# Kernel optimization log

Measured on AMD Instinct MI355X. Metric: run time of the kernel, lower is better.

## Reference

```python
import jax, jax.numpy as jnp
import numpy as np

D = 256      # d_model
H = 8        # num heads
HD = D // H  # head dim
DFF = 1024   # feedforward dim
S = 1024     # seq len
B = 8        # batch
EPS = 1e-5


def _layernorm(x, g, b):
    mu = jnp.mean(x, axis=-1, keepdims=True)
    var = jnp.mean((x - mu) ** 2, axis=-1, keepdims=True)
    return (x - mu) * jax.lax.rsqrt(var + EPS) * g + b


def setup_inputs() -> dict:
    key = jax.random.key(0)
    ks = jax.random.split(key, 12)
    xav = lambda k, shape: jax.random.uniform(
        k, shape, jnp.float32, -1.0, 1.0) * np.sqrt(6.0 / (shape[0] + shape[-1]))
    return {
        "src": jax.random.normal(ks[0], (S, B, D), jnp.float32),
        "bias": jax.random.normal(ks[1], (B, H, S, S), jnp.float32),
        "in_proj_w": xav(ks[2], (3 * D, D)),
        "in_proj_b": jnp.zeros((3 * D,), jnp.float32),
        "out_w": xav(ks[3], (D, D)),
        "out_b": jnp.zeros((D,), jnp.float32),
        "w1": xav(ks[4], (DFF, D)),
        "b1": jnp.zeros((DFF,), jnp.float32),
        "w2": xav(ks[5], (D, DFF)),
        "b2": jnp.zeros((D,), jnp.float32),
        "g1": jnp.ones((D,), jnp.float32),
        "be1": jnp.zeros((D,), jnp.float32),
        "g2": jnp.ones((D,), jnp.float32),
        "be2": jnp.zeros((D,), jnp.float32),
    }


def reference(src, bias, in_proj_w, in_proj_b, out_w, out_b,
              w1, b1, w2, b2, g1, be1, g2, be2):
    # Pre-norm (note: residual uses the NORMED src, matching the torch code)
    x = _layernorm(src, g1, be1)                       # [S,B,D]
    qkv = x @ in_proj_w.T + in_proj_b                  # [S,B,3D]
    q, k, v = jnp.split(qkv, 3, axis=-1)
    q = q * (HD ** -0.5)
    # [S,B,D] -> [B,H,S,HD]
    to_heads = lambda t: t.reshape(S, B, H, HD).transpose(1, 2, 0, 3)
    qh, kh, vh = to_heads(q), to_heads(k), to_heads(v)
    scores = jnp.einsum('bhsd,bhtd->bhst', qh, kh) + bias
    attn = jax.nn.softmax(scores, axis=-1)             # [B,H,S,S]
    ctx = jnp.einsum('bhst,bhtd->bhsd', attn, vh)      # [B,H,S,HD]
    ctx = ctx.transpose(2, 0, 1, 3).reshape(S, B, D)
    attn_out = ctx @ out_w.T + out_b
    x = x + attn_out                                   # residual (eval: no dropout)
    y = _layernorm(x, g2, be2)
    ff = jax.nn.relu(y @ w1.T + b1) @ w2.T + b2
    return y + ff
```

## Files before the change

### kernel.cpp

```cpp
#include <hip/hip_runtime.h>
#include <hip/hip_bf16.h>
#include <cstdint>

typedef unsigned short u16;
typedef __attribute__((ext_vector_type(8))) short bf16x8;
typedef __attribute__((ext_vector_type(4))) float f32x4;

#define S_LEN 1024
#define BATCH 8
#define DMODEL 256
#define NHEAD 8
#define HDIM 32
#define DFF 1024
#define NROWS (S_LEN * BATCH)

static __device__ __forceinline__ u16 f2b(float f) {
    union { float f; unsigned u; } x{f};
    unsigned r = (x.u + 0x7fffu + ((x.u >> 16) & 1u)) >> 16;
    return (u16)r;
}
static __device__ __forceinline__ float b2f(unsigned h) {
    union { unsigned u; float f; } x{h << 16};
    return x.f;
}

__global__ __launch_bounds__(256) void prep_kernel(
    const float* __restrict__ in, const float* __restrict__ g1,
    const float* __restrict__ be1, u16* __restrict__ ob,
    const float* __restrict__ ipw, const float* __restrict__ outw,
    const float* __restrict__ w1, const float* __restrict__ w2,
    const float* __restrict__ ipb,
    u16* __restrict__ wqkv, u16* __restrict__ wout,
    u16* __restrict__ w1b, u16* __restrict__ w2b, float* __restrict__ bq)
{
    const float s = 0.17677669529663689f;
    if (blockIdx.x >= 2048) {
        const int i4 = ((int)blockIdx.x - 2048) * 1024 + threadIdx.x * 4;
        const float* src; u16* dst; int off; float sc = 1.0f;
        if (i4 < 196608)      { src = ipw;  dst = wqkv; off = 0;      if (i4 < 65536) sc = s; }
        else if (i4 < 262144) { src = outw; dst = wout; off = 196608; }
        else if (i4 < 524288) { src = w1;   dst = w1b;  off = 262144; }
        else                  { src = w2;   dst = w2b;  off = 524288; }
        const float4 v = *(const float4*)(src + i4 - off);
        uint2 pk;
        pk.x = (unsigned)f2b(v.x * sc) | ((unsigned)f2b(v.y * sc) << 16);
        pk.y = (unsigned)f2b(v.z * sc) | ((unsigned)f2b(v.w * sc) << 16);
        *(uint2*)(dst + i4 - off) = pk;
        if (i4 < 768) {
            const float4 b = *(const float4*)(ipb + i4);
            const float bs = (i4 < 256) ? s : 1.0f;
            *(float4*)(bq + i4) = make_float4(b.x * bs, b.y * bs, b.z * bs, b.w * bs);
        }
        return;
    }
    const int w = threadIdx.x >> 6, l = threadIdx.x & 63;
    const int row = blockIdx.x * 4 + w;
    const float4 v = *(const float4*)(in + (size_t)row * DMODEL + l * 4);
    float s0 = v.x + v.y + v.z + v.w;
    #pragma unroll
    for (int o = 32; o; o >>= 1) s0 += __shfl_xor(s0, o);
    const float mu = s0 * (1.0f / DMODEL);
    const float dx = v.x - mu, dy = v.y - mu, dz = v.z - mu, dw = v.w - mu;
    float sq = dx * dx + dy * dy + dz * dz + dw * dw;
    #pragma unroll
    for (int o = 32; o; o >>= 1) sq += __shfl_xor(sq, o);
    const float rs = rsqrtf(sq * (1.0f / DMODEL) + 1e-5f);
    const float4 gv = *(const float4*)(g1 + l * 4);
    const float4 bv = *(const float4*)(be1 + l * 4);
    const float r0 = dx * rs * gv.x + bv.x;
    const float r1 = dy * rs * gv.y + bv.y;
    const float r2 = dz * rs * gv.z + bv.z;
    const float r3 = dw * rs * gv.w + bv.w;
    uint2 pk;
    pk.x = (unsigned)f2b(r0) | ((unsigned)f2b(r1) << 16);
    pk.y = (unsigned)f2b(r2) | ((unsigned)f2b(r3) << 16);
    *(uint2*)(ob + (size_t)row * DMODEL + l * 4) = pk;
}

template <int MF, int NF>
__device__ __forceinline__ void gemm_core(
    const u16* __restrict__ A, const u16* __restrict__ Bw,
    int K, int nbase, int rowbase, u16* sB, f32x4 acc[MF][NF])
{
    const int tid = threadIdx.x, w = tid >> 6, l = tid & 63;
    const int g = l >> 4, q = l & 15;
    const u16* Arow = A + (size_t)(rowbase + w * (MF * 16) + q) * K + g * 8;

    const int sbr = tid >> 3, sseg = tid & 7;
    const int LOADS = NF / 2;
    const int CHUNK = NF * 16 * 128;
    size_t bsrc[LOADS];
    int d[LOADS];
    #pragma unroll
    for (int i = 0; i < LOADS; ++i) {
        bsrc[i] = (size_t)(nbase + sbr + 32 * i) * K + sseg * 8;
        d[i] = (sbr + 32 * i) * 128 + ((sseg * 16) ^ ((sbr & 7) << 4));
    }

    {
        #pragma unroll
        for (int i = 0; i < LOADS; ++i) {
            const uint4 r = *(const uint4*)(Bw + bsrc[i]);
            *(uint4*)((char*)sB + d[i]) = r;
        }
    }
    const int NC = K >> 6;
    for (int c = 0; c < NC; ++c) {
        __syncthreads();
        char* sBc = (char*)sB + (c & 1) * CHUNK;
        char* sBn = (char*)sB + ((c + 1) & 1) * CHUNK;
        uint4 p[LOADS];
        if (c + 1 < NC) {
            #pragma unroll
            for (int i = 0; i < LOADS; ++i)
                p[i] = *(const uint4*)(Bw + bsrc[i] + (c + 1) * 64);
        }
        const int kk = c * 64;
        #pragma unroll
        for (int ks = 0; ks < 2; ++ks) {
            bf16x8 af[MF];
            #pragma unroll
            for (int m = 0; m < MF; ++m)
                af[m] = *(const bf16x8*)(Arow + (size_t)m * 16 * K + kk + ks * 32);
            #pragma unroll
            for (int n = 0; n < NF; ++n) {
                const int rr = n * 16 + q;
                const bf16x8 bf = *(const bf16x8*)(
                    sBc + rr * 128 + ((ks * 64 + g * 16) ^ ((rr & 7) << 4)));
                #pragma unroll
                for (int m = 0; m < MF; ++m)
                    acc[m][n] = __builtin_amdgcn_mfma_f32_16x16x32_bf16(bf, af[m], acc[m][n], 0, 0, 0);
            }
        }
        if (c + 1 < NC) {
            #pragma unroll
            for (int i = 0; i < LOADS; ++i)
                *(uint4*)(sBn + d[i]) = p[i];
        }
    }
}

__global__ __launch_bounds__(256) void gemm_qkv(
    const u16* __restrict__ A, const u16* __restrict__ Bw,
    const float* __restrict__ bias,
    u16* __restrict__ Qh, u16* __restrict__ Kh, u16* __restrict__ Vt)
{
    __shared__ u16 sB[2][128 * 64];
    const int tid = threadIdx.x, w = tid >> 6, l = tid & 63;
    const int g = l >> 4, q = l & 15;
    const int rowbase = blockIdx.x * 128, nbase = blockIdx.y * 128;
    f32x4 acc[2][8] = {};
    gemm_core<2, 8>(A, Bw, 256, nbase, rowbase, &sB[0][0], acc);

    #pragma unroll
    for (int m = 0; m < 2; ++m) {
        const int row = rowbase + w * 32 + m * 16 + q;
        const int s = row >> 3, b = row & 7;
        #pragma unroll
        for (int n = 0; n < 8; ++n) {
            const int col = nbase + n * 16 + g * 4;
            const float4 bv = *(const float4*)(bias + col);
            if (col < 512) {
                u16* dst = (col >= 256) ? Kh : Qh;
                const int cc = col & 255, h = cc >> 5, hd = cc & 31;
                const int bh = b * 8 + h;
                uint2 pk;
                pk.x = (unsigned)f2b(acc[m][n][0] + bv.x) | ((unsigned)f2b(acc[m][n][1] + bv.y) << 16);
                pk.y = (unsigned)f2b(acc[m][n][2] + bv.z) | ((unsigned)f2b(acc[m][n][3] + bv.w) << 16);
                *(uint2*)(dst + ((size_t)bh * S_LEN + s) * HDIM + hd) = pk;
            } else {
                const int cc = col - 512, h = cc >> 5, hd = cc & 31;
                const int bh = b * 8 + h;
                Vt[((size_t)bh * HDIM + hd + 0) * S_LEN + s] = f2b(acc[m][n][0] + bv.x);
                Vt[((size_t)bh * HDIM + hd + 1) * S_LEN + s] = f2b(acc[m][n][1] + bv.y);
                Vt[((size_t)bh * HDIM + hd + 2) * S_LEN + s] = f2b(acc[m][n][2] + bv.z);
                Vt[((size_t)bh * HDIM + hd + 3) * S_LEN + s] = f2b(acc[m][n][3] + bv.w);
            }
        }
    }
}

__global__ __launch_bounds__(256) void gemm_ffn1(
    const u16* __restrict__ A, const u16* __restrict__ Bw,
    const float* __restrict__ bias, u16* __restrict__ outb)
{
    __shared__ u16 sB[2][128 * 64];
    const int tid = threadIdx.x, w = tid >> 6, l = tid & 63;
    const int g = l >> 4, q = l & 15;
    const int rowbase = blockIdx.x * 128, nbase = blockIdx.y * 128;
    f32x4 acc[2][8] = {};
    gemm_core<2, 8>(A, Bw, 256, nbase, rowbase, &sB[0][0], acc);

    #pragma unroll
    for (int m = 0; m < 2; ++m) {
        const int row = rowbase + w * 32 + m * 16 + q;
        #pragma unroll
        for (int n = 0; n < 8; ++n) {
            const int col = nbase + n * 16 + g * 4;
            const float4 bv = *(const float4*)(bias + col);
            const float v0 = fmaxf(acc[m][n][0] + bv.x, 0.f);
            const float v1 = fmaxf(acc[m][n][1] + bv.y, 0.f);
            const float v2 = fmaxf(acc[m][n][2] + bv.z, 0.f);
            const float v3 = fmaxf(acc[m][n][3] + bv.w, 0.f);
            uint2 pk;
            pk.x = (unsigned)f2b(v0) | ((unsigned)f2b(v1) << 16);
            pk.y = (unsigned)f2b(v2) | ((unsigned)f2b(v3) << 16);
            *(uint2*)(outb + (size_t)row * DFF + col) = pk;
        }
    }
}

__global__ __launch_bounds__(256) void gemm_ffn2(
    const u16* __restrict__ A, const u16* __restrict__ Bw,
    const float* __restrict__ bias, const u16* __restrict__ resid,
    float* __restrict__ outf)
{
    __shared__ u16 sB[2][64 * 64];
    const int tid = threadIdx.x, w = tid >> 6, l = tid & 63;
    const int g = l >> 4, q = l & 15;
    const int rowbase = blockIdx.x * 128, nbase = blockIdx.y * 64;
    f32x4 acc[2][4] = {};
    gemm_core<2, 4>(A, Bw, 1024, nbase, rowbase, &sB[0][0], acc);

    #pragma unroll
    for (int m = 0; m < 2; ++m) {
        const int row = rowbase + w * 32 + m * 16 + q;
        #pragma unroll
        for (int n = 0; n < 4; ++n) {
            const int col = nbase + n * 16 + g * 4;
            const float4 bv = *(const float4*)(bias + col);
            const uint2 rp = *(const uint2*)(resid + (size_t)row * DMODEL + col);
            *(float4*)(outf + (size_t)row * DMODEL + col) = make_float4(
                acc[m][n][0] + bv.x + b2f(rp.x & 0xffffu),
                acc[m][n][1] + bv.y + b2f(rp.x >> 16),
                acc[m][n][2] + bv.z + b2f(rp.y & 0xffffu),
                acc[m][n][3] + bv.w + b2f(rp.y >> 16));
        }
    }
}

__global__ __launch_bounds__(256) void attn_kernel(
    const u16* __restrict__ Qh, const u16* __restrict__ Kh,
    const u16* __restrict__ Vt, const float* __restrict__ bias,
    u16* __restrict__ ctx)
{
    __shared__ u16 sK[2][64 * 32];
    __shared__ u16 sV[2][32 * 64];
    __shared__ u16 sP[4][16 * 64];
    const int tid = threadIdx.x, w = tid >> 6, l = tid & 63;
    const int g = l >> 4, q = l & 15;
    const int bh = blockIdx.x, b = bh >> 3, h = bh & 7;
    const int qbase = blockIdx.y * 64 + w * 16;
    const int qrow = qbase + q;

    const bf16x8 qf = *(const bf16x8*)(Qh + ((size_t)bh * S_LEN + qrow) * HDIM + g * 8);
    const float* brow = bias + ((size_t)bh * S_LEN + qrow) * S_LEN;
    u16* Pw = sP[w];
    const int swz = (q & 7) << 4;

    const u16* KsrcBase = Kh + ((size_t)bh * S_LEN + w * 16 + q) * HDIM + g * 8;
    const u16* VsrcBase = Vt + ((size_t)bh * HDIM + (w & 1) * 16 + q) * S_LEN
                             + (w >> 1) * 32 + g * 8;
    u16* KdstA = &sK[0][tid * 8]; u16* KdstB = &sK[1][tid * 8];
    u16* VdstA = &sV[0][tid * 8]; u16* VdstB = &sV[1][tid * 8];

    f32x4 ctxa[2] = {{0,0,0,0},{0,0,0,0}};
    float m = -1e30f, lsum = 0.f;

    auto loadB = [&](int kt, f32x4* bv) {
        #pragma unroll
        for (int n = 0; n < 4; ++n)
            bv[n] = __builtin_nontemporal_load(
                (const f32x4*)(brow + kt * 64 + n * 16 + g * 4));
    };

    auto proc = [&](int buf, const f32x4* bv) {
        f32x4 sc[4];
        #pragma unroll
        for (int n = 0; n < 4; ++n) {
            const bf16x8 kf = *(const bf16x8*)(&sK[buf][(n * 64 + l) * 8]);
            f32x4 z = {0, 0, 0, 0};
            sc[n] = __builtin_amdgcn_mfma_f32_16x16x32_bf16(kf, qf, z, 0, 0, 0);
        }
        #pragma unroll
        for (int n = 0; n < 4; ++n)
            #pragma unroll
            for (int r = 0; r < 4; ++r) sc[n][r] += bv[n][r];

        float mx = sc[0][0];
        #pragma unroll
        for (int n = 0; n < 4; ++n)
            #pragma unroll
            for (int r = 0; r < 4; ++r) mx = fmaxf(mx, sc[n][r]);
        mx = fmaxf(mx, __shfl_xor(mx, 16));
        mx = fmaxf(mx, __shfl_xor(mx, 32));
        const float mn = fmaxf(m, mx);
        const float corr = __expf(m - mn);
        float su = 0.f;
        u16 pb[16];
        #pragma unroll
        for (int n = 0; n < 4; ++n)
            #pragma unroll
            for (int r = 0; r < 4; ++r) {
                const float pv = __expf(sc[n][r] - mn);
                su += pv;
                pb[n * 4 + r] = f2b(pv);
            }
        su += __shfl_xor(su, 16);
        su += __shfl_xor(su, 32);
        lsum = lsum * corr + su;
        m = mn;
        #pragma unroll
        for (int jg = 0; jg < 2; ++jg)
            #pragma unroll
            for (int r = 0; r < 4; ++r) ctxa[jg][r] *= corr;

        #pragma unroll
        for (int n = 0; n < 4; ++n) {
            uint2 pk;
            pk.x = (unsigned)pb[n * 4] | ((unsigned)pb[n * 4 + 1] << 16);
            pk.y = (unsigned)pb[n * 4 + 2] | ((unsigned)pb[n * 4 + 3] << 16);
            *(uint2*)((char*)Pw + q * 128 + ((n * 32 + g * 8) ^ swz)) = pk;
        }

        #pragma unroll
        for (int ks = 0; ks < 2; ++ks) {
            const bf16x8 pf = *(const bf16x8*)((char*)Pw + q * 128 + ((ks * 64 + g * 16) ^ swz));
            #pragma unroll
            for (int jg = 0; jg < 2; ++jg) {
                const bf16x8 vf = *(const bf16x8*)(&sV[buf][((ks * 2 + jg) * 64 + l) * 8]);
                ctxa[jg] = __builtin_amdgcn_mfma_f32_16x16x32_bf16(vf, pf, ctxa[jg], 0, 0, 0);
            }
        }
    };

    f32x4 bv0[4], bv1[4];
    {
        const uint4 kr = *(const uint4*)(KsrcBase);
        const uint4 vr = *(const uint4*)(VsrcBase);
        *(uint4*)KdstA = kr;
        *(uint4*)VdstA = vr;
        loadB(0, bv0);
    }
    __syncthreads();

    for (int kt = 0; kt < 16; kt += 2) {
        {
            uint4 kr, vr;
            kr = *(const uint4*)(KsrcBase + (size_t)(kt + 1) * 64 * HDIM);
            vr = *(const uint4*)(VsrcBase + (size_t)(kt + 1) * 64);
            loadB(kt + 1, bv1);
            proc(0, bv0);
            *(uint4*)KdstB = kr;
            *(uint4*)VdstB = vr;
        }
        __syncthreads();
        {
            uint4 kr, vr;
            if (kt + 2 < 16) {
                kr = *(const uint4*)(KsrcBase + (size_t)(kt + 2) * 64 * HDIM);
                vr = *(const uint4*)(VsrcBase + (size_t)(kt + 2) * 64);
                loadB(kt + 2, bv0);
            }
            proc(1, bv1);
            if (kt + 2 < 16) {
                *(uint4*)KdstA = kr;
                *(uint4*)VdstA = vr;
            }
        }
        __syncthreads();
    }

    const float inv = 1.0f / lsum;
    #pragma unroll
    for (int jg = 0; jg < 2; ++jg) {
        uint2 pk;
        pk.x = (unsigned)f2b(ctxa[jg][0] * inv) | ((unsigned)f2b(ctxa[jg][1] * inv) << 16);
        pk.y = (unsigned)f2b(ctxa[jg][2] * inv) | ((unsigned)f2b(ctxa[jg][3] * inv) << 16);
        *(uint2*)(ctx + ((size_t)qrow * 8 + b) * DMODEL + h * 32 + jg * 16 + g * 4) = pk;
    }
}

__global__ __launch_bounds__(256) void oproj_ln(
    const u16* __restrict__ ctx, const u16* __restrict__ wob,
    const float* __restrict__ ob, const u16* __restrict__ xb,
    const float* __restrict__ g2, const float* __restrict__ be2,
    u16* __restrict__ yb)
{
    __shared__ float s1[4][32], s2[4][32];
    const int tid = threadIdx.x, wv = tid >> 6, l = tid & 63;
    const int g = l >> 4, q = l & 15;
    const int rowbase = blockIdx.x * 32;
    f32x4 acc[2][4] = {};
    const u16* Arow = ctx + (size_t)(rowbase + q) * 256 + g * 8;
    const u16* Brow = wob + (size_t)(wv * 64 + q) * 256 + g * 8;

    #pragma unroll 2
    for (int kk = 0; kk < 256; kk += 32) {
        bf16x8 af[2];
        #pragma unroll
        for (int m = 0; m < 2; ++m)
            af[m] = *(const bf16x8*)(Arow + (size_t)m * 16 * 256 + kk);
        #pragma unroll
        for (int n = 0; n < 4; ++n) {
            const bf16x8 bf = *(const bf16x8*)(Brow + (size_t)n * 16 * 256 + kk);
            #pragma unroll
            for (int m = 0; m < 2; ++m)
                acc[m][n] = __builtin_amdgcn_mfma_f32_16x16x32_bf16(bf, af[m], acc[m][n], 0, 0, 0);
        }
    }

    float sum[2] = {0.f, 0.f};
    #pragma unroll
    for (int m = 0; m < 2; ++m) {
        const int row = rowbase + m * 16 + q;
        #pragma unroll
        for (int n = 0; n < 4; ++n) {
            const int col = wv * 64 + n * 16 + g * 4;
            const float4 bv = *(const float4*)(ob + col);
            const uint2 rp = *(const uint2*)(xb + (size_t)row * 256 + col);
            acc[m][n][0] += bv.x + b2f(rp.x & 0xffffu);
            acc[m][n][1] += bv.y + b2f(rp.x >> 16);
            acc[m][n][2] += bv.z + b2f(rp.y & 0xffffu);
            acc[m][n][3] += bv.w + b2f(rp.y >> 16);
            sum[m] += acc[m][n][0] + acc[m][n][1] + acc[m][n][2] + acc[m][n][3];
        }
        sum[m] += __shfl_xor(sum[m], 16);
        sum[m] += __shfl_xor(sum[m], 32);
    }
    if (l < 16) { s1[wv][q] = sum[0]; s1[wv][16 + q] = sum[1]; }
    __syncthreads();
    float mu[2], rs[2];
    #pragma unroll
    for (int m = 0; m < 2; ++m) {
        const int lr = m * 16 + q;
        mu[m] = (s1[0][lr] + s1[1][lr] + s1[2][lr] + s1[3][lr]) * (1.0f / 256);
    }
    float sq[2] = {0.f, 0.f};
    #pragma unroll
    for (int m = 0; m < 2; ++m) {
        #pragma unroll
        for (int n = 0; n < 4; ++n)
            #pragma unroll
            for (int r = 0; r < 4; ++r) {
                const float d = acc[m][n][r] - mu[m];
                sq[m] += d * d;
            }
        sq[m] += __shfl_xor(sq[m], 16);
        sq[m] += __shfl_xor(sq[m], 32);
    }
    if (l < 16) { s2[wv][q] = sq[0]; s2[wv][16 + q] = sq[1]; }
    __syncthreads();
    #pragma unroll
    for (int m = 0; m < 2; ++m) {
        const int lr = m * 16 + q;
        rs[m] = rsqrtf((s2[0][lr] + s2[1][lr] + s2[2][lr] + s2[3][lr]) * (1.0f / 256) + 1e-5f);
    }

    #pragma unroll
    for (int m = 0; m < 2; ++m) {
        const int row = rowbase + m * 16 + q;
        #pragma unroll
        for (int n = 0; n < 4; ++n) {
            const int col = wv * 64 + n * 16 + g * 4;
            const float4 gv = *(const float4*)(g2 + col);
            const float4 b2 = *(const float4*)(be2 + col);
            const float y0 = (acc[m][n][0] - mu[m]) * rs[m] * gv.x + b2.x;
            const float y1 = (acc[m][n][1] - mu[m]) * rs[m] * gv.y + b2.y;
            const float y2 = (acc[m][n][2] - mu[m]) * rs[m] * gv.z + b2.z;
            const float y3 = (acc[m][n][3] - mu[m]) * rs[m] * gv.w + b2.w;
            uint2 pk;
            pk.x = (unsigned)f2b(y0) | ((unsigned)f2b(y1) << 16);
            pk.y = (unsigned)f2b(y2) | ((unsigned)f2b(y3) << 16);
            *(uint2*)(yb + (size_t)row * 256 + col) = pk;
        }
    }
}

extern "C" void kernel_launch(void* const* d_in, const int* in_sizes, int n_in,
                              void* d_out, int out_size, void* d_ws, size_t ws_size,
                              hipStream_t stream)
{
    const float* src  = (const float*)d_in[0];
    const float* bias = (const float*)d_in[1];
    const float* ipw  = (const float*)d_in[2];
    const float* ipb  = (const float*)d_in[3];
    const float* outw = (const float*)d_in[4];
    const float* outb = (const float*)d_in[5];
    const float* w1   = (const float*)d_in[6];
    const float* b1   = (const float*)d_in[7];
    const float* w2   = (const float*)d_in[8];
    const float* b2   = (const float*)d_in[9];
    const float* g1   = (const float*)d_in[10];
    const float* be1  = (const float*)d_in[11];
    const float* g2   = (const float*)d_in[12];
    const float* be2  = (const float*)d_in[13];

    char* p = (char*)d_ws;
    auto alloc = [&](size_t bytes) -> void* {
        void* r = (void*)p;
        p += (bytes + 255) & ~(size_t)255;
        return r;
    };
    u16*   xb   = (u16*)  alloc((size_t)NROWS * DMODEL * 2);
    u16*   Qh   = (u16*)  alloc((size_t)64 * S_LEN * HDIM * 2);
    u16*   Kb   = (u16*)  alloc((size_t)64 * S_LEN * HDIM * 2);
    u16*   Vt   = (u16*)  alloc((size_t)64 * S_LEN * HDIM * 2);
    u16*   ctx  = (u16*)  alloc((size_t)NROWS * DMODEL * 2);
    u16*   yb   = (u16*)  alloc((size_t)NROWS * DMODEL * 2);
    u16*   hb   = (u16*)  alloc((size_t)NROWS * DFF * 2);
    u16*   wqkv = (u16*)  alloc((size_t)768 * 256 * 2);
    u16*   wob  = (u16*)  alloc((size_t)256 * 256 * 2);
    u16*   w1b  = (u16*)  alloc((size_t)1024 * 256 * 2);
    u16*   w2b  = (u16*)  alloc((size_t)256 * 1024 * 2);
    float* bq   = (float*)alloc(768 * 4);

    prep_kernel<<<2816, 256, 0, stream>>>(src, g1, be1, xb,
                                          ipw, outw, w1, w2, ipb,
                                          wqkv, wob, w1b, w2b, bq);
    gemm_qkv<<<dim3(64, 6), 256, 0, stream>>>(xb, wqkv, bq, Qh, Kb, Vt);
    attn_kernel<<<dim3(64, 16), 256, 0, stream>>>(Qh, Kb, Vt, bias, ctx);
    oproj_ln<<<256, 256, 0, stream>>>(ctx, wob, outb, xb, g2, be2, yb);
    gemm_ffn1<<<dim3(64, 8), 256, 0, stream>>>(yb, w1b, b1, hb);
    gemm_ffn2<<<dim3(64, 4), 256, 0, stream>>>(hb, w2b, b2, yb, (float*)d_out);
}
```

Baseline: 152.5 us.

## Load K/V fragments directly from global memory instead of shared-memory staging

The attention kernel no longer stages K and V tiles through double-buffered shared memory. Each wave now reads its MFMA K and V fragments straight from global memory, which removes the LDS stores and the two __syncthreads per iteration. The cost is that all four waves redundantly load the same K/V data, relying on L1/L2 hits, and global load latency is exposed inside proc without explicit prefetching.

```diff
diff --git a/kernel.cpp b/kernel.cpp
--- a/kernel.cpp
+++ b/kernel.cpp
@@ -244,8 +244,6 @@
     const u16* __restrict__ Vt, const float* __restrict__ bias,
     u16* __restrict__ ctx)
 {
-    __shared__ u16 sK[2][64 * 32];
-    __shared__ u16 sV[2][32 * 64];
     __shared__ u16 sP[4][16 * 64];
     const int tid = threadIdx.x, w = tid >> 6, l = tid & 63;
     const int g = l >> 4, q = l & 15;
@@ -258,11 +256,8 @@
     u16* Pw = sP[w];
     const int swz = (q & 7) << 4;
 
-    const u16* KsrcBase = Kh + ((size_t)bh * S_LEN + w * 16 + q) * HDIM + g * 8;
-    const u16* VsrcBase = Vt + ((size_t)bh * HDIM + (w & 1) * 16 + q) * S_LEN
-                             + (w >> 1) * 32 + g * 8;
-    u16* KdstA = &sK[0][tid * 8]; u16* KdstB = &sK[1][tid * 8];
-    u16* VdstA = &sV[0][tid * 8]; u16* VdstB = &sV[1][tid * 8];
+    const u16* Kfr = Kh + ((size_t)bh * S_LEN + q) * HDIM + g * 8;
+    const u16* Vfr = Vt + ((size_t)bh * HDIM + q) * S_LEN + g * 8;
 
     f32x4 ctxa[2] = {{0,0,0,0},{0,0,0,0}};
     float m = -1e30f, lsum = 0.f;
@@ -274,13 +269,23 @@
                 (const f32x4*)(brow + kt * 64 + n * 16 + g * 4));
     };
 
-    auto proc = [&](int buf, const f32x4* bv) {
+    auto proc = [&](int kt, const f32x4* bv) {
+        bf16x8 kf[4];
+        #pragma unroll
+        for (int n = 0; n < 4; ++n)
+            kf[n] = *(const bf16x8*)(Kfr + (size_t)(kt * 64 + n * 16) * HDIM);
+        bf16x8 vf[2][2];
+        #pragma unroll
+        for (int ks = 0; ks < 2; ++ks)
+            #pragma unroll
+            for (int jg = 0; jg < 2; ++jg)
+                vf[ks][jg] = *(const bf16x8*)(Vfr + (size_t)jg * 16 * S_LEN + kt * 64 + ks * 32);
+
         f32x4 sc[4];
         #pragma unroll
         for (int n = 0; n < 4; ++n) {
-            const bf16x8 kf = *(const bf16x8*)(&sK[buf][(n * 64 + l) * 8]);
             f32x4 z = {0, 0, 0, 0};
-            sc[n] = __builtin_amdgcn_mfma_f32_16x16x32_bf16(kf, qf, z, 0, 0, 0);
+            sc[n] = __builtin_amdgcn_mfma_f32_16x16x32_bf16(kf[n], qf, z, 0, 0, 0);
         }
         #pragma unroll
         for (int n = 0; n < 4; ++n)
@@ -327,48 +332,18 @@
         for (int ks = 0; ks < 2; ++ks) {
             const bf16x8 pf = *(const bf16x8*)((char*)Pw + q * 128 + ((ks * 64 + g * 16) ^ swz));
             #pragma unroll
-            for (int jg = 0; jg < 2; ++jg) {
-                const bf16x8 vf = *(const bf16x8*)(&sV[buf][((ks * 2 + jg) * 64 + l) * 8]);
-                ctxa[jg] = __builtin_amdgcn_mfma_f32_16x16x32_bf16(vf, pf, ctxa[jg], 0, 0, 0);
-            }
+            for (int jg = 0; jg < 2; ++jg)
+                ctxa[jg] = __builtin_amdgcn_mfma_f32_16x16x32_bf16(vf[ks][jg], pf, ctxa[jg], 0, 0, 0);
         }
     };
 
-    f32x4 bv0[4], bv1[4];
-    {
-        const uint4 kr = *(const uint4*)(KsrcBase);
-        const uint4 vr = *(const uint4*)(VsrcBase);
-        *(uint4*)KdstA = kr;
-        *(uint4*)VdstA = vr;
-        loadB(0, bv0);
-    }
-    __syncthreads();
-
+    f32x4 bvA[4], bvB[4];
+    loadB(0, bvA);
     for (int kt = 0; kt < 16; kt += 2) {
-        {
-            uint4 kr, vr;
-            kr = *(const uint4*)(KsrcBase + (size_t)(kt + 1) * 64 * HDIM);
-            vr = *(const uint4*)(VsrcBase + (size_t)(kt + 1) * 64);
-            loadB(kt + 1, bv1);
-            proc(0, bv0);
-            *(uint4*)KdstB = kr;
-            *(uint4*)VdstB = vr;
-        }
-        __syncthreads();
-        {
-            uint4 kr, vr;
-            if (kt + 2 < 16) {
-                kr = *(const uint4*)(KsrcBase + (size_t)(kt + 2) * 64 * HDIM);
-                vr = *(const uint4*)(VsrcBase + (size_t)(kt + 2) * 64);
-                loadB(kt + 2, bv0);
-            }
-            proc(1, bv1);
-            if (kt + 2 < 16) {
-                *(uint4*)KdstA = kr;
-                *(uint4*)VdstA = vr;
-            }
-        }
-        __syncthreads();
+        loadB(kt + 1, bvB);
+        proc(kt, bvA);
+        if (kt + 2 < 16) loadB(kt + 2, bvA);
+        proc(kt + 1, bvB);
     }
 
     const float inv = 1.0f / lsum;
```

Measured after the change: 167.5 us. +9.9%, slower.
